# Optimization experiments

Measured on AMD Instinct MI355X. Metric: run time of the kernel, lower is better.

## Reference

```python
import jax, jax.numpy as jnp
import numpy as np

B = 64
H_FS = W_FS = 56
IN_DIM, OUT_DIM, NUM_HEADS = 96, 192, 2
HEAD_DIM = OUT_DIM // NUM_HEADS  # 96
STRIDE_Q, STRIDE_KV = (2, 2), (4, 4)
REL_RANGE = 2 * (H_FS // STRIDE_Q[0]) - 1  # 55
LN_EPS = 1e-5


def setup_inputs() -> dict:
    key = jax.random.key(0)
    ks = jax.random.split(key, 12)
    N = H_FS * W_FS + 1  # +1 cls token
    s = 0.02
    d = {
        "hidden_states": jax.random.normal(ks[0], (B, N, IN_DIM), jnp.float32),
        "Wq": jax.random.normal(ks[1], (IN_DIM, OUT_DIM), jnp.float32) * s,
        "bq": jnp.zeros((OUT_DIM,), jnp.float32),
        "Wk": jax.random.normal(ks[2], (IN_DIM, OUT_DIM), jnp.float32) * s,
        "bk": jnp.zeros((OUT_DIM,), jnp.float32),
        "Wv": jax.random.normal(ks[3], (IN_DIM, OUT_DIM), jnp.float32) * s,
        "bv": jnp.zeros((OUT_DIM,), jnp.float32),
        # depthwise pool convs: (C_out=C, C_in/groups=1, kh, kw)
        "pool_q_w": jax.random.normal(ks[4], (IN_DIM, 1, 3, 3), jnp.float32) * 0.1,
        "pool_k_w": jax.random.normal(ks[5], (IN_DIM, 1, 3, 3), jnp.float32) * 0.1,
        "pool_v_w": jax.random.normal(ks[6], (IN_DIM, 1, 3, 3), jnp.float32) * 0.1,
        "gq": jnp.ones((IN_DIM,), jnp.float32), "betaq": jnp.zeros((IN_DIM,), jnp.float32),
        "gk": jnp.ones((IN_DIM,), jnp.float32), "betak": jnp.zeros((IN_DIM,), jnp.float32),
        "gv": jnp.ones((IN_DIM,), jnp.float32), "betav": jnp.zeros((IN_DIM,), jnp.float32),
        "rel_h": jax.random.normal(ks[7], (REL_RANGE, HEAD_DIM), jnp.float32) * s,
        "rel_w": jax.random.normal(ks[8], (REL_RANGE, HEAD_DIM), jnp.float32) * s,
        "height": H_FS,
        "width": W_FS,
    }
    return d


def _layernorm(x, g, b):
    m = x.mean(-1, keepdims=True)
    v = ((x - m) ** 2).mean(-1, keepdims=True)
    return (x - m) * jax.lax.rsqrt(v + LN_EPS) * g + b


def _pool(x, w, stride, g, b, height, width):
    # x: (B, folds=1, N, C) with cls token first
    bsz, _, _, C = x.shape
    cls_tok, rest = x[:, :, :1], x[:, :, 1:]
    sp = rest.reshape(bsz, height, width, C).transpose(0, 3, 1, 2)  # (B, C, H, W)
    y = jax.lax.conv_general_dilated(
        sp, w, stride, [(1, 1), (1, 1)], feature_group_count=C,
        dimension_numbers=("NCHW", "OIHW", "NCHW"))
    hp, wp = y.shape[2], y.shape[3]
    y = y.reshape(bsz, 1, C, hp * wp).transpose(0, 1, 3, 2)  # (B, 1, N', C)
    y = jnp.concatenate([cls_tok, y], axis=2)
    return _layernorm(y, g, b), (hp, wp)


def _rel_idx(qn, kn):
    q_ratio = max(kn / qn, 1.0)
    k_ratio = max(qn / kn, 1.0)
    dist = (np.arange(qn)[:, None] * q_ratio - np.arange(kn)[None, :] * k_ratio
            + (kn - 1) * k_ratio)
    return dist.astype(np.int64)


def reference(hidden_states, Wq, bq, Wk, bk, Wv, bv, pool_q_w, pool_k_w, pool_v_w,
              gq, betaq, gk, betak, gv, betav, rel_h, rel_w, height, width):
    bsz, N, C = hidden_states.shape
    h = hidden_states.reshape(bsz, N, 1, C).transpose(0, 2, 1, 3)  # (B, folds=1, N, C)

    q, (qh, qw) = _pool(h, pool_q_w, STRIDE_Q, gq, betaq, height, width)
    k, (kh, kw) = _pool(h, pool_k_w, STRIDE_KV, gk, betak, height, width)
    v, _ = _pool(h, pool_v_w, STRIDE_KV, gv, betav, height, width)

    def proj(x, W, bias, n):
        x = x.transpose(0, 2, 1, 3).reshape(bsz, n, -1)
        x = x @ W + bias
        return x.reshape(bsz, n, NUM_HEADS, HEAD_DIM).transpose(0, 2, 1, 3)

    nq, nk = qh * qw + 1, kh * kw + 1
    q = proj(q, Wq, bq, nq)  # (B, H, nq, d)
    k = proj(k, Wk, bk, nk)
    v = proj(v, Wv, bv, nk)

    scale = HEAD_DIM ** -0.5
    attn = jnp.einsum("bhqd,bhkd->bhqk", q * scale, k)

    # decomposed spatial relative positional bias (cls offset = 1)
    Rh = rel_h[_rel_idx(qh, kh)]  # (qh, kh, d)
    Rw = rel_w[_rel_idx(qw, kw)]  # (qw, kw, d)
    rq = q[:, :, 1:].reshape(bsz, NUM_HEADS, qh, qw, HEAD_DIM)
    eh = jnp.einsum("byhwc,hkc->byhwk", rq, Rh)
    ew = jnp.einsum("byhwc,wkc->byhwk", rq, Rw)
    blk = (attn[:, :, 1:, 1:].reshape(bsz, NUM_HEADS, qh, qw, kh, kw)
           + eh[..., :, None] + ew[..., None, :])
    attn = attn.at[:, :, 1:, 1:].set(blk.reshape(bsz, NUM_HEADS, qh * qw, kh * kw))

    attn = jax.nn.softmax(attn, axis=-1)
    out = jnp.einsum("bhqk,bhkd->bhqd", attn, v)
    out = out.at[:, :, 1:].add(q[:, :, 1:])  # residual pooling (skip cls)
    return out.transpose(0, 2, 1, 3).reshape(bsz, nq, OUT_DIM)
```

## Files before the change

kernel.cpp:

```cpp
#include <hip/hip_runtime.h>
#include <hip/hip_bf16.h>
#include <hip/hip_fp16.h>

#define B_    64
#define HFS   56
#define CIN   96
#define NQ    785
#define NK    197
#define QW    28
#define KW    14
#define NTOT  3137
#define NQP   800
#define NKP   208
#define NKPV  224
#define VROWS 112
#define KSCL  0.10206207261596575f
#define LOG2E 1.4426950408889634f
#define KSCL2 (KSCL*LOG2E)

typedef __attribute__((ext_vector_type(8))) short short8;
typedef __attribute__((ext_vector_type(4))) short shortx4;
typedef __attribute__((ext_vector_type(4))) float floatx4;

__device__ __forceinline__ short f2s(float x) {
    __hip_bfloat16 h = __float2bfloat16(x);
    return *reinterpret_cast<short*>(&h);
}
__device__ __forceinline__ float s2f(short s) {
    __hip_bfloat16 h; *reinterpret_cast<short*>(&h) = s;
    return __bfloat162float(h);
}
__device__ __forceinline__ short8 ld8(const short* p) {
    return *reinterpret_cast<const short8*>(p);
}
__device__ __forceinline__ unsigned pkbf(float a, float b) {
    return (unsigned)(unsigned short)f2s(a) | ((unsigned)(unsigned short)f2s(b) << 16);
}
__device__ __forceinline__ unsigned pkhf(float a, float b) {
    __half2 h = __floats2half2_rn(a, b);
    return *reinterpret_cast<unsigned*>(&h);
}
__device__ __forceinline__ float hflo(unsigned w) {
    __half2 h = *reinterpret_cast<__half2*>(&w);
    return __half2float(__low2half(h));
}
__device__ __forceinline__ float hfhi(unsigned w) {
    __half2 h = *reinterpret_cast<__half2*>(&w);
    return __half2float(__high2half(h));
}

#define MFMA16(a,b,c) __builtin_amdgcn_mfma_f32_16x16x32_bf16((a),(b),(c),0,0,0)

__global__ void prep_kernel(const float* __restrict__ Wq, const float* __restrict__ Wk,
                            const float* __restrict__ Wv, const float* __restrict__ relh,
                            const float* __restrict__ relw,
                            const float* __restrict__ pqw, const float* __restrict__ pkw,
                            const float* __restrict__ pvw,
                            short* __restrict__ WTq, short* __restrict__ WTk,
                            short* __restrict__ WTv, short* __restrict__ relc,
                            short* __restrict__ vt,
                            float* __restrict__ cwqT, float* __restrict__ cwkT,
                            float* __restrict__ cwvT)
{
    int i = blockIdx.x * 256 + threadIdx.x;
    if (i < 18432)      { int o = i/96, c = i%96;              WTq[o*96+c] = f2s(Wq[c*192+o]); }
    else if (i < 36864) { int j = i-18432; int o=j/96,c=j%96;  WTk[o*96+c] = f2s(Wk[c*192+o]*KSCL2); }
    else if (i < 55296) { int j = i-36864; int o=j/96,c=j%96;  WTv[o*96+c] = f2s(Wv[c*192+o]); }
    else if (i < 66048) {
        int j = i - 55296;  int r = j/96, c = j%96;
        float v = (r < 54) ? relh[r*96+c] : ((r < 108) ? relw[(r-54)*96+c] : 0.f);
        relc[r*96+c] = f2s(v*LOG2E);
    } else if (i < 721408) {
        int j2 = i - 66048;
        int bh = j2 / 5120, r = j2 % 5120;
        int row, tok; short val;
        if (r < 3584) { row = 96 + r/224; tok = r%224;
                        val = (row == 96 && tok < NK) ? (short)0x3F80 : (short)0; }
        else          { int rr = r-3584; row = rr/16; tok = 208 + (rr%16); val = 0; }
        vt[((long)bh*VROWS + row)*NKPV + tok] = val;
    } else if (i < 724000) {
        int j = i - 721408;
        int w = j / 864, r = j % 864;
        int c = r / 9, off = r % 9;
        const float* src = (w == 0) ? pqw : (w == 1) ? pkw : pvw;
        float*       dst = (w == 0) ? cwqT : (w == 1) ? cwkT : cwvT;
        dst[off*96 + c] = src[c*9 + off];
    }
}

__device__ __forceinline__ void red16_2(float& s, float& ss) {
    #pragma unroll
    for (int off = 8; off >= 1; off >>= 1) {
        s  += __shfl_xor(s,  off, 16);
        ss += __shfl_xor(ss, off, 16);
    }
}

__device__ __forceinline__ void ln6_store(const float* x, float m, float r,
    const float* __restrict__ g, const float* __restrict__ beta,
    int c0, short* __restrict__ outp)
{
    float2 g0 = *reinterpret_cast<const float2*>(g + c0);
    float2 g1 = *reinterpret_cast<const float2*>(g + c0 + 2);
    float2 g2 = *reinterpret_cast<const float2*>(g + c0 + 4);
    float2 b0 = *reinterpret_cast<const float2*>(beta + c0);
    float2 b1 = *reinterpret_cast<const float2*>(beta + c0 + 2);
    float2 b2 = *reinterpret_cast<const float2*>(beta + c0 + 4);
    unsigned o0 = pkbf((x[0]-m)*r*g0.x + b0.x, (x[1]-m)*r*g0.y + b0.y);
    unsigned o1 = pkbf((x[2]-m)*r*g1.x + b1.x, (x[3]-m)*r*g1.y + b1.y);
    unsigned o2 = pkbf((x[4]-m)*r*g2.x + b2.x, (x[5]-m)*r*g2.y + b2.y);
    *reinterpret_cast<unsigned*>(outp)     = o0;
    *reinterpret_cast<unsigned*>(outp + 2) = o1;
    *reinterpret_cast<unsigned*>(outp + 4) = o2;
}

__device__ __forceinline__ void zero6(short* __restrict__ outp) {
    *reinterpret_cast<unsigned*>(outp)     = 0u;
    *reinterpret_cast<unsigned*>(outp + 2) = 0u;
    *reinterpret_cast<unsigned*>(outp + 4) = 0u;
}

__global__ __launch_bounds__(256) void pool_ln_kernel(
    const float* __restrict__ hs,
    const float* __restrict__ cwqT, const float* __restrict__ cwkT, const float* __restrict__ cwvT,
    const float* __restrict__ gq, const float* __restrict__ betaq,
    const float* __restrict__ gk, const float* __restrict__ betak,
    const float* __restrict__ gv, const float* __restrict__ betav,
    short* __restrict__ pq, short* __restrict__ pk, short* __restrict__ pv)
{
    const int wid  = threadIdx.x >> 6;
    const int lane = threadIdx.x & 63;
    const int sub  = lane >> 4;
    const int li   = lane & 15;
    const int c0   = li * 6;
    const int gid  = blockIdx.x * 4 + wid;
    const int b    = gid / 252;
    const int slot = gid % 252;
    const long hb  = (long)b * NTOT * CIN;

    if (slot < 200) {
        int t = slot*4 + sub;
        short* outp = pq + ((long)b*NQP + t)*CIN + c0;
        if (t >= NQ) { zero6(outp); return; }
        float x[6];
        #pragma unroll
        for (int i = 0; i < 6; ++i) x[i] = 0.f;
        if (t == 0) {
            const float* hp = hs + hb + c0;
            float2 a0 = *reinterpret_cast<const float2*>(hp);
            float2 a1 = *reinterpret_cast<const float2*>(hp + 2);
            float2 a2 = *reinterpret_cast<const float2*>(hp + 4);
            x[0]=a0.x; x[1]=a0.y; x[2]=a1.x; x[3]=a1.y; x[4]=a2.x; x[5]=a2.y;
        } else {
            int j = t - 1, oy = j / QW, ox = j % QW;
            float2 hbuf[9][3];
            #pragma unroll
            for (int tap = 0; tap < 9; ++tap) {
                int dy = tap / 3, dx = tap % 3;
                int iy = oy*2 - 1 + dy;
                int ix = ox*2 - 1 + dx;
                if (iy >= 0 && iy < HFS && ix >= 0 && ix < HFS) {
                    const float* hp = hs + hb + (long)(1 + iy*HFS + ix)*CIN + c0;
                    hbuf[tap][0] = *reinterpret_cast<const float2*>(hp);
                    hbuf[tap][1] = *reinterpret_cast<const float2*>(hp + 2);
                    hbuf[tap][2] = *reinterpret_cast<const float2*>(hp + 4);
                } else {
                    hbuf[tap][0] = float2{0.f, 0.f};
                    hbuf[tap][1] = float2{0.f, 0.f};
                    hbuf[tap][2] = float2{0.f, 0.f};
                }
            }
            #pragma unroll
            for (int tap = 0; tap < 9; ++tap) {
                const float* wp = cwqT + tap*96 + c0;
                float2 w0 = *reinterpret_cast<const float2*>(wp);
                float2 w1 = *reinterpret_cast<const float2*>(wp + 2);
                float2 w2 = *reinterpret_cast<const float2*>(wp + 4);
                x[0] = fmaf(hbuf[tap][0].x, w0.x, x[0]); x[1] = fmaf(hbuf[tap][0].y, w0.y, x[1]);
                x[2] = fmaf(hbuf[tap][1].x, w1.x, x[2]); x[3] = fmaf(hbuf[tap][1].y, w1.y, x[3]);
                x[4] = fmaf(hbuf[tap][2].x, w2.x, x[4]); x[5] = fmaf(hbuf[tap][2].y, w2.y, x[5]);
            }
        }
        float s  = (x[0]+x[1]) + (x[2]+x[3]) + (x[4]+x[5]);
        float ss = fmaf(x[0],x[0], fmaf(x[1],x[1], fmaf(x[2],x[2],
                   fmaf(x[3],x[3], fmaf(x[4],x[4], x[5]*x[5])))));
        red16_2(s, ss);
        float m   = s * (1.f/96.f);
        float var = ss * (1.f/96.f) - m*m;
        float r   = rsqrtf(var + 1e-5f);
        ln6_store(x, m, r, gq, betaq, c0, outp);
    } else {
        int tok = (slot - 200)*4 + sub;
        short* ok_ = pk + ((long)b*NKP + tok)*CIN + c0;
        short* ov_ = pv + ((long)b*NKP + tok)*CIN + c0;
        if (tok >= NK) { zero6(ok_); zero6(ov_); return; }
        float xk[6], xv[6];
        #pragma unroll
        for (int i = 0; i < 6; ++i) { xk[i] = 0.f; xv[i] = 0.f; }
        if (tok == 0) {
            const float* hp = hs + hb + c0;
            float2 a0 = *reinterpret_cast<const float2*>(hp);
            float2 a1 = *reinterpret_cast<const float2*>(hp + 2);
            float2 a2 = *reinterpret_cast<const float2*>(hp + 4);
            xk[0]=xv[0]=a0.x; xk[1]=xv[1]=a0.y; xk[2]=xv[2]=a1.x;
            xk[3]=xv[3]=a1.y; xk[4]=xv[4]=a2.x; xk[5]=xv[5]=a2.y;
        } else {
            int j = tok - 1, oy = j / KW, ox = j % KW;
            float2 hbuf[9][3];
            #pragma unroll
            for (int tap = 0; tap < 9; ++tap) {
                int dy = tap / 3, dx = tap % 3;
                int iy = oy*4 - 1 + dy;
                int ix = ox*4 - 1 + dx;
                if (iy >= 0 && iy < HFS && ix >= 0 && ix < HFS) {
                    const float* hp = hs + hb + (long)(1 + iy*HFS + ix)*CIN + c0;
                    hbuf[tap][0] = *reinterpret_cast<const float2*>(hp);
                    hbuf[tap][1] = *reinterpret_cast<const float2*>(hp + 2);
                    hbuf[tap][2] = *reinterpret_cast<const float2*>(hp + 4);
                } else {
                    hbuf[tap][0] = float2{0.f, 0.f};
                    hbuf[tap][1] = float2{0.f, 0.f};
                    hbuf[tap][2] = float2{0.f, 0.f};
                }
            }
            #pragma unroll
            for (int tap = 0; tap < 9; ++tap) {
                int wo = tap*96 + c0;
                float2 k0 = *reinterpret_cast<const float2*>(cwkT + wo);
                float2 k1 = *reinterpret_cast<const float2*>(cwkT + wo + 2);
                float2 k2 = *reinterpret_cast<const float2*>(cwkT + wo + 4);
                float2 v0 = *reinterpret_cast<const float2*>(cwvT + wo);
                float2 v1 = *reinterpret_cast<const float2*>(cwvT + wo + 2);
                float2 v2 = *reinterpret_cast<const float2*>(cwvT + wo + 4);
                xk[0] = fmaf(hbuf[tap][0].x, k0.x, xk[0]); xk[1] = fmaf(hbuf[tap][0].y, k0.y, xk[1]);
                xk[2] = fmaf(hbuf[tap][1].x, k1.x, xk[2]); xk[3] = fmaf(hbuf[tap][1].y, k1.y, xk[3]);
                xk[4] = fmaf(hbuf[tap][2].x, k2.x, xk[4]); xk[5] = fmaf(hbuf[tap][2].y, k2.y, xk[5]);
                xv[0] = fmaf(hbuf[tap][0].x, v0.x, xv[0]); xv[1] = fmaf(hbuf[tap][0].y, v0.y, xv[1]);
                xv[2] = fmaf(hbuf[tap][1].x, v1.x, xv[2]); xv[3] = fmaf(hbuf[tap][1].y, v1.y, xv[3]);
                xv[4] = fmaf(hbuf[tap][2].x, v2.x, xv[4]); xv[5] = fmaf(hbuf[tap][2].y, v2.y, xv[5]);
            }
        }
        float sk  = (xk[0]+xk[1]) + (xk[2]+xk[3]) + (xk[4]+xk[5]);
        float ssk = fmaf(xk[0],xk[0], fmaf(xk[1],xk[1], fmaf(xk[2],xk[2],
                    fmaf(xk[3],xk[3], fmaf(xk[4],xk[4], xk[5]*xk[5])))));
        float sv  = (xv[0]+xv[1]) + (xv[2]+xv[3]) + (xv[4]+xv[5]);
        float ssv = fmaf(xv[0],xv[0], fmaf(xv[1],xv[1], fmaf(xv[2],xv[2],
                    fmaf(xv[3],xv[3], fmaf(xv[4],xv[4], xv[5]*xv[5])))));
        red16_2(sk, ssk);
        red16_2(sv, ssv);
        float mk = sk * (1.f/96.f), vark = ssk * (1.f/96.f) - mk*mk;
        float mv = sv * (1.f/96.f), varv = ssv * (1.f/96.f) - mv*mv;
        float rk = rsqrtf(vark + 1e-5f);
        float rv = rsqrtf(varv + 1e-5f);
        ln6_store(xk, mk, rk, gk, betak, c0, ok_);
        ln6_store(xv, mv, rv, gv, betav, c0, ov_);
    }
}

__global__ __launch_bounds__(256) void proj_mfma_kernel(
    const short* __restrict__ pq, const short* __restrict__ pk, const short* __restrict__ pv,
    const short* __restrict__ WTq, const short* __restrict__ WTk, const short* __restrict__ WTv,
    const float* __restrict__ bq, const float* __restrict__ bk, const float* __restrict__ bv,
    short* __restrict__ qb, short* __restrict__ kb, short* __restrict__ vt)
{
    int wid  = threadIdx.x >> 6;
    int lane = threadIdx.x & 63;
    int quad = lane >> 4, col = lane & 15;
    int wt = blockIdx.x * 4 + wid;

    if (wt < 1008) {
        const short *A, *WT; const float* bias; short* outp;
        int ntokp, row0; float bsc;
        if (wt < 800) { A = pq; WT = WTq; bias = bq; outp = qb; ntokp = NQP; row0 = wt*64; bsc = 1.f; }
        else          { A = pk; WT = WTk; bias = bk; outp = kb; ntokp = NKP; row0 = (wt-800)*64; bsc = KSCL2; }

        short8 bt[4][3];
        #pragma unroll
        for (int ti = 0; ti < 4; ++ti)
            #pragma unroll
            for (int cc = 0; cc < 3; ++cc)
                bt[ti][cc] = ld8(A + (long)(row0 + ti*16 + col)*96 + cc*32 + quad*8);

        int bT[4], tokT[4];
        #pragma unroll
        for (int ti = 0; ti < 4; ++ti) {
            int r = row0 + ti*16;
            bT[ti] = r / ntokp;
            tokT[ti] = (r % ntokp) + col;
        }

        short8 af[2][3];
        #pragma unroll
        for (int cc = 0; cc < 3; ++cc)
            af[0][cc] = ld8(WT + col*96 + cc*32 + quad*8);

        #pragma unroll
        for (int nt = 0; nt < 12; ++nt) {
            if (nt < 11) {
                #pragma unroll
                for (int cc = 0; cc < 3; ++cc)
                    af[(nt+1)&1][cc] = ld8(WT + ((nt+1)*16 + col)*96 + cc*32 + quad*8);
            }
            int o0 = nt*16 + quad*4;
            float4 bo = *reinterpret_cast<const float4*>(bias + o0);
            int h  = (o0 >= 96) ? 1 : 0;
            int d0 = o0 - h*96;
            #pragma unroll
            for (int ti = 0; ti < 4; ++ti) {
                floatx4 acc = {0.f, 0.f, 0.f, 0.f};
                #pragma unroll
                for (int cc = 0; cc < 3; ++cc)
                    acc = MFMA16(af[nt&1][cc], bt[ti][cc], acc);
                shortx4 val;
                val.x = f2s(acc[0] + bo.x*bsc);
                val.y = f2s(acc[1] + bo.y*bsc);
                val.z = f2s(acc[2] + bo.z*bsc);
                val.w = f2s(acc[3] + bo.w*bsc);
                *reinterpret_cast<shortx4*>(outp + ((long)(bT[ti]*2 + h)*ntokp + tokT[ti])*96 + d0) = val;
            }
        }
    } else {
        int row0 = (wt - 1008) * 64;
        short8 at[4][3];
        #pragma unroll
        for (int ti = 0; ti < 4; ++ti)
            #pragma unroll
            for (int cc = 0; cc < 3; ++cc)
                at[ti][cc] = ld8(pv + (long)(row0 + ti*16 + col)*96 + cc*32 + quad*8);

        int bT[4], t0T[4];
        #pragma unroll
        for (int ti = 0; ti < 4; ++ti) {
            int r = row0 + ti*16;
            bT[ti] = r / NKP;
            t0T[ti] = (r % NKP) + quad*4;
        }

        short8 bf[2][3];
        #pragma unroll
        for (int cc = 0; cc < 3; ++cc)
            bf[0][cc] = ld8(WTv + col*96 + cc*32 + quad*8);

        #pragma unroll
        for (int nt = 0; nt < 12; ++nt) {
            if (nt < 11) {
                #pragma unroll
                for (int cc = 0; cc < 3; ++cc)
                    bf[(nt+1)&1][cc] = ld8(WTv + ((nt+1)*16 + col)*96 + cc*32 + quad*8);
            }
            int o = nt*16 + col;
            int h = (o >= 96) ? 1 : 0;
            int d = o - h*96;
            float bo = bv[o];
            #pragma unroll
            for (int ti = 0; ti < 4; ++ti) {
                floatx4 acc = {0.f, 0.f, 0.f, 0.f};
                #pragma unroll
                for (int cc = 0; cc < 3; ++cc)
                    acc = MFMA16(at[ti][cc], bf[nt&1][cc], acc);
                shortx4 val;
                val.x = (t0T[ti]+0 < NK) ? f2s(acc[0] + bo) : (short)0;
                val.y = (t0T[ti]+1 < NK) ? f2s(acc[1] + bo) : (short)0;
                val.z = (t0T[ti]+2 < NK) ? f2s(acc[2] + bo) : (short)0;
                val.w = (t0T[ti]+3 < NK) ? f2s(acc[3] + bo) : (short)0;
                *reinterpret_cast<shortx4*>(vt + ((long)(bT[ti]*2 + h)*VROWS + d)*NKPV + t0T[ti]) = val;
            }
        }
    }
}

__global__ __launch_bounds__(64, 2) void attn_kernel(
    const short* __restrict__ qb, const short* __restrict__ kb,
    const short* __restrict__ vt, const short* __restrict__ relc,
    float* __restrict__ out)
{
    __shared__ __align__(16) short smem[2][16][232];

    int lane = threadIdx.x & 63;
    int quad = lane >> 4, col = lane & 15;

    int bid = blockIdx.x;
    int wt  = (bid & 7) * 400 + (bid >> 3);
    int bh  = wt / 25;
    int tp  = wt % 25;
    int q0  = tp * 32;

    const short* qrow = qb + ((long)bh*NQP + q0)*96;
    short8 aq[2][3];
    #pragma unroll
    for (int ti = 0; ti < 2; ++ti)
        #pragma unroll
        for (int c = 0; c < 3; ++c)
            aq[ti][c] = ld8(qrow + (ti*16 + col)*96 + c*32 + quad*8);

    short8 rf[2][3];
    #pragma unroll
    for (int c = 0; c < 3; ++c)
        rf[0][c] = ld8(relc + col*96 + c*32 + quad*8);
    #pragma unroll
    for (int rt = 0; rt < 7; ++rt) {
        if (rt < 6) {
            #pragma unroll
            for (int c = 0; c < 3; ++c)
                rf[(rt+1)&1][c] = ld8(relc + ((rt+1)*16 + col)*96 + c*32 + quad*8);
        }
        #pragma unroll
        for (int ti = 0; ti < 2; ++ti) {
            floatx4 acc = {0.f, 0.f, 0.f, 0.f};
            #pragma unroll
            for (int c = 0; c < 3; ++c)
                acc = MFMA16(aq[ti][c], rf[rt&1][c], acc);
            #pragma unroll
            for (int reg = 0; reg < 4; ++reg)
                smem[ti][quad*4 + reg][rt*16 + col] = f2s(acc[reg]);
        }
    }

    const short* kbase = kb + (long)bh*NKP*96;
    short8 kf[3][3];
    #pragma unroll
    for (int c = 0; c < 3; ++c)
        kf[0][c] = ld8(kbase + col*96 + c*32 + quad*8);
    #pragma unroll
    for (int c = 0; c < 3; ++c)
        kf[1][c] = ld8(kbase + (16 + col)*96 + c*32 + quad*8);

    int qyo[2][4], qxo[2][4];
    #pragma unroll
    for (int ti = 0; ti < 2; ++ti)
        #pragma unroll
        for (int reg = 0; reg < 4; ++reg) {
            int qq = q0 + ti*16 + quad*4 + reg;
            int jj = (qq > 0) ? (qq - 1) : 0;
            qyo[ti][reg] = jj / QW;
            qxo[ti][reg] = jj % QW;
        }

    unsigned bpk[2][13][2];
    #pragma unroll
    for (int kt = 0; kt < 13; ++kt) {
        int k  = kt*16 + col;
        int kk = (k > 0) ? (k - 1) : 0;
        int ky = kk / 14;  ky = (ky < 13) ? ky : 13;
        int kx = kk - 14*ky;
        int oh  = 26 - 2*ky;
        int ow2 = 26 - 2*kx;
        #pragma unroll
        for (int ti = 0; ti < 2; ++ti) {
            float bs[4];
            #pragma unroll
            for (int reg = 0; reg < 4; ++reg) {
                const short* er = &smem[ti][quad*4 + reg][0];
                float bias = s2f(er[qyo[ti][reg] + oh]) + s2f(er[54 + qxo[ti][reg] + ow2]);
                if (kt == 0) bias = (col == 0) ? 0.f : bias;
                if (q0 == 0 && ti == 0 && reg == 0) bias = (quad == 0) ? 0.f : bias;
                bs[reg] = bias;
            }
            bpk[ti][kt][0] = pkhf(bs[0], bs[1]);
            bpk[ti][kt][1] = pkhf(bs[2], bs[3]);
        }
    }

    const short* vbase = vt + (long)bh*VROWS*NKPV;
    short8 vf[2][7];
    #pragma unroll
    for (int kt = 0; kt < 13; ++kt) {
        if (kt < 11) {
            #pragma unroll
            for (int c = 0; c < 3; ++c)
                kf[(kt+2)%3][c] = ld8(kbase + ((kt+2)*16 + col)*96 + c*32 + quad*8);
        } else if (kt == 11) {
            #pragma unroll
            for (int nt = 0; nt < 7; ++nt)
                vf[0][nt] = ld8(vbase + (nt*16 + col)*NKPV + quad*8);
        }
        int k = kt*16 + col;
        __builtin_amdgcn_s_setprio(1);
        floatx4 accA = {0.f, 0.f, 0.f, 0.f};
        floatx4 accB = {0.f, 0.f, 0.f, 0.f};
        #pragma unroll
        for (int c = 0; c < 3; ++c) {
            accA = MFMA16(aq[0][c], kf[kt%3][c], accA);
            accB = MFMA16(aq[1][c], kf[kt%3][c], accB);
        }
        __builtin_amdgcn_s_setprio(0);
        unsigned a0 = bpk[0][kt][0], a1 = bpk[0][kt][1];
        unsigned b0 = bpk[1][kt][0], b1 = bpk[1][kt][1];
        smem[0][quad*4 + 0][k] = f2s(__builtin_amdgcn_exp2f(accA[0] + hflo(a0)));
        smem[0][quad*4 + 1][k] = f2s(__builtin_amdgcn_exp2f(accA[1] + hfhi(a0)));
        smem[0][quad*4 + 2][k] = f2s(__builtin_amdgcn_exp2f(accA[2] + hflo(a1)));
        smem[0][quad*4 + 3][k] = f2s(__builtin_amdgcn_exp2f(accA[3] + hfhi(a1)));
        smem[1][quad*4 + 0][k] = f2s(__builtin_amdgcn_exp2f(accB[0] + hflo(b0)));
        smem[1][quad*4 + 1][k] = f2s(__builtin_amdgcn_exp2f(accB[1] + hfhi(b0)));
        smem[1][quad*4 + 2][k] = f2s(__builtin_amdgcn_exp2f(accB[2] + hflo(b1)));
        smem[1][quad*4 + 3][k] = f2s(__builtin_amdgcn_exp2f(accB[3] + hfhi(b1)));
    }
    #pragma unroll
    for (int ti = 0; ti < 2; ++ti)
        #pragma unroll
        for (int reg = 0; reg < 4; ++reg)
            smem[ti][quad*4 + reg][208 + col] = 0;

    floatx4 o[2][7];
    #pragma unroll
    for (int ti = 0; ti < 2; ++ti)
        #pragma unroll
        for (int nt = 0; nt < 7; ++nt) o[ti][nt] = floatx4{0.f, 0.f, 0.f, 0.f};
    #pragma unroll
    for (int c = 0; c < 7; ++c) {
        if (c < 6) {
            #pragma unroll
            for (int nt = 0; nt < 7; ++nt)
                vf[(c+1)&1][nt] = ld8(vbase + (nt*16 + col)*NKPV + (c+1)*32 + quad*8);
        }
        short8 apA = ld8(&smem[0][col][c*32 + quad*8]);
        short8 apB = ld8(&smem[1][col][c*32 + quad*8]);
        __builtin_amdgcn_s_setprio(1);
        #pragma unroll
        for (int nt = 0; nt < 7; ++nt) {
            o[0][nt] = MFMA16(apA, vf[c&1][nt], o[0][nt]);
            o[1][nt] = MFMA16(apB, vf[c&1][nt], o[1][nt]);
        }
        __builtin_amdgcn_s_setprio(0);
    }

    float inv[2][4];
    #pragma unroll
    for (int ti = 0; ti < 2; ++ti)
        #pragma unroll
        for (int reg = 0; reg < 4; ++reg) {
            float srow = __shfl(o[ti][6][reg], lane & 48, 64);
            inv[ti][reg] = 1.0f / srow;
        }

    float* fsm = reinterpret_cast<float*>(&smem[0][0][0]);
    #pragma unroll
    for (int ti = 0; ti < 2; ++ti)
        #pragma unroll
        for (int nt = 0; nt < 6; ++nt)
            #pragma unroll
            for (int reg = 0; reg < 4; ++reg)
                fsm[(ti*16 + quad*4 + reg)*102 + nt*16 + col] = o[ti][nt][reg] * inv[ti][reg];

    int b = bh >> 1, h = bh & 1;
    int r2  = lane >> 1;
    int h2  = lane & 1;
    int ti2 = r2 >> 4, row2 = r2 & 15;
    int q   = q0 + ti2*16 + row2;
    int ch0 = h2 * 48;
    if (q < NQ) {
        const float* src  = fsm + (ti2*16 + row2)*102 + ch0;
        const short* resp = qb + ((long)bh*NQP + q)*96 + ch0;
        float*       outp = out + ((long)b*NQ + q)*192 + h*96 + ch0;
        #pragma unroll
        for (int i = 0; i < 6; ++i) {
            float2 v0 = *reinterpret_cast<const float2*>(src + i*8 + 0);
            float2 v1 = *reinterpret_cast<const float2*>(src + i*8 + 2);
            float2 v2 = *reinterpret_cast<const float2*>(src + i*8 + 4);
            float2 v3 = *reinterpret_cast<const float2*>(src + i*8 + 6);
            float r_[8];
            if (q > 0) {
                short8 rs = ld8(resp + i*8);
                #pragma unroll
                for (int j = 0; j < 8; ++j) r_[j] = s2f(rs[j]);
            } else {
                #pragma unroll
                for (int j = 0; j < 8; ++j) r_[j] = 0.f;
            }
            float4 o0, o1;
            o0.x = v0.x + r_[0]; o0.y = v0.y + r_[1];
            o0.z = v1.x + r_[2]; o0.w = v1.y + r_[3];
            o1.x = v2.x + r_[4]; o1.y = v2.y + r_[5];
            o1.z = v3.x + r_[6]; o1.w = v3.y + r_[7];
            *reinterpret_cast<float4*>(outp + i*8)     = o0;
            *reinterpret_cast<float4*>(outp + i*8 + 4) = o1;
        }
    }
}

extern "C" void kernel_launch(void* const* d_in, const int* in_sizes, int n_in,
                              void* d_out, int out_size, void* d_ws, size_t ws_size,
                              hipStream_t stream)
{
    const float* hs    = (const float*)d_in[0];
    const float* Wq    = (const float*)d_in[1];
    const float* bq    = (const float*)d_in[2];
    const float* Wk    = (const float*)d_in[3];
    const float* bk    = (const float*)d_in[4];
    const float* Wv    = (const float*)d_in[5];
    const float* bv    = (const float*)d_in[6];
    const float* pqw   = (const float*)d_in[7];
    const float* pkw   = (const float*)d_in[8];
    const float* pvw   = (const float*)d_in[9];
    const float* gq    = (const float*)d_in[10];
    const float* betaq = (const float*)d_in[11];
    const float* gk    = (const float*)d_in[12];
    const float* betak = (const float*)d_in[13];
    const float* gv    = (const float*)d_in[14];
    const float* betav = (const float*)d_in[15];
    const float* relh  = (const float*)d_in[16];
    const float* relw  = (const float*)d_in[17];
    float* out = (float*)d_out;

    short* pq   = (short*)d_ws;
    short* pk   = pq  + (long)B_*NQP*CIN;
    short* pv   = pk  + (long)B_*NKP*CIN;
    short* qb   = pv  + (long)B_*NKP*CIN;
    short* kb   = qb  + (long)128*NQP*96;
    short* vt   = kb  + (long)128*NKP*96;
    short* WTq  = vt  + (long)128*VROWS*NKPV;
    short* WTk  = WTq + 192*96;
    short* WTv  = WTk + 192*96;
    short* relc = WTv + 192*96;
    float* cwqT = (float*)(relc + 112*96);
    float* cwkT = cwqT + 9*96;
    float* cwvT = cwkT + 9*96;

    prep_kernel<<<2829, 256, 0, stream>>>(Wq, Wk, Wv, relh, relw,
                                          pqw, pkw, pvw,
                                          WTq, WTk, WTv, relc, vt,
                                          cwqT, cwkT, cwvT);

    pool_ln_kernel<<<(B_*1008)/16, 256, 0, stream>>>(
        hs, cwqT, cwkT, cwvT, gq, betaq, gk, betak, gv, betav, pq, pk, pv);

    proj_mfma_kernel<<<1216/4, 256, 0, stream>>>(
        pq, pk, pv, WTq, WTk, WTv, bq, bk, bv, qb, kb, vt);

    attn_kernel<<<3200, 64, 0, stream>>>(qb, kb, vt, relc, out);
}
```

Baseline: 233.9 us.

## Fold weight prep into pool kernel and widen pool/LN loads to 8 channels

The large prep kernel is split up. The conv-weight transpose stays in a tiny 11-block kernel, while the projection-weight transpose, relative-bias conversion and vt padding init move into extra blocks appended to the pool/LN launch. The vt init now writes short8 vectors instead of single shorts. The pool/LN path switches from 6 channels per lane to 8 channels with float4 loads and 16-byte stores, leaving 4 of every 16 lanes idle. The aim is to cut launch count and per-element memory ops, at the cost of lane underutilisation and some divergence in the pool kernel.

```diff
diff --git a/kernel.cpp b/kernel.cpp
--- a/kernel.cpp
+++ b/kernel.cpp
@@ -21,6 +21,7 @@
 typedef __attribute__((ext_vector_type(8))) short short8;
 typedef __attribute__((ext_vector_type(4))) short shortx4;
 typedef __attribute__((ext_vector_type(4))) float floatx4;
+typedef __attribute__((ext_vector_type(4))) unsigned uintx4;
 
 __device__ __forceinline__ short f2s(float x) {
     __hip_bfloat16 h = __float2bfloat16(x);
@@ -51,36 +52,14 @@
 
 #define MFMA16(a,b,c) __builtin_amdgcn_mfma_f32_16x16x32_bf16((a),(b),(c),0,0,0)
 
-__global__ void prep_kernel(const float* __restrict__ Wq, const float* __restrict__ Wk,
-                            const float* __restrict__ Wv, const float* __restrict__ relh,
-                            const float* __restrict__ relw,
-                            const float* __restrict__ pqw, const float* __restrict__ pkw,
-                            const float* __restrict__ pvw,
-                            short* __restrict__ WTq, short* __restrict__ WTk,
-                            short* __restrict__ WTv, short* __restrict__ relc,
-                            short* __restrict__ vt,
-                            float* __restrict__ cwqT, float* __restrict__ cwkT,
-                            float* __restrict__ cwvT)
+__global__ void prep_w_kernel(const float* __restrict__ pqw, const float* __restrict__ pkw,
+                              const float* __restrict__ pvw,
+                              float* __restrict__ cwqT, float* __restrict__ cwkT,
+                              float* __restrict__ cwvT)
 {
     int i = blockIdx.x * 256 + threadIdx.x;
-    if (i < 18432)      { int o = i/96, c = i%96;              WTq[o*96+c] = f2s(Wq[c*192+o]); }
-    else if (i < 36864) { int j = i-18432; int o=j/96,c=j%96;  WTk[o*96+c] = f2s(Wk[c*192+o]*KSCL2); }
-    else if (i < 55296) { int j = i-36864; int o=j/96,c=j%96;  WTv[o*96+c] = f2s(Wv[c*192+o]); }
-    else if (i < 66048) {
-        int j = i - 55296;  int r = j/96, c = j%96;
-        float v = (r < 54) ? relh[r*96+c] : ((r < 108) ? relw[(r-54)*96+c] : 0.f);
-        relc[r*96+c] = f2s(v*LOG2E);
-    } else if (i < 721408) {
-        int j2 = i - 66048;
-        int bh = j2 / 5120, r = j2 % 5120;
-        int row, tok; short val;
-        if (r < 3584) { row = 96 + r/224; tok = r%224;
-                        val = (row == 96 && tok < NK) ? (short)0x3F80 : (short)0; }
-        else          { int rr = r-3584; row = rr/16; tok = 208 + (rr%16); val = 0; }
-        vt[((long)bh*VROWS + row)*NKPV + tok] = val;
-    } else if (i < 724000) {
-        int j = i - 721408;
-        int w = j / 864, r = j % 864;
+    if (i < 2592) {
+        int w = i / 864, r = i % 864;
         int c = r / 9, off = r % 9;
         const float* src = (w == 0) ? pqw : (w == 1) ? pkw : pvw;
         float*       dst = (w == 0) ? cwqT : (w == 1) ? cwkT : cwvT;
@@ -96,28 +75,25 @@
     }
 }
 
-__device__ __forceinline__ void ln6_store(const float* x, float m, float r,
+__device__ __forceinline__ void ln8_store(const float* x, float m, float r,
     const float* __restrict__ g, const float* __restrict__ beta,
     int c0, short* __restrict__ outp)
 {
-    float2 g0 = *reinterpret_cast<const float2*>(g + c0);
-    float2 g1 = *reinterpret_cast<const float2*>(g + c0 + 2);
-    float2 g2 = *reinterpret_cast<const float2*>(g + c0 + 4);
-    float2 b0 = *reinterpret_cast<const float2*>(beta + c0);
-    float2 b1 = *reinterpret_cast<const float2*>(beta + c0 + 2);
-    float2 b2 = *reinterpret_cast<const float2*>(beta + c0 + 4);
-    unsigned o0 = pkbf((x[0]-m)*r*g0.x + b0.x, (x[1]-m)*r*g0.y + b0.y);
-    unsigned o1 = pkbf((x[2]-m)*r*g1.x + b1.x, (x[3]-m)*r*g1.y + b1.y);
-    unsigned o2 = pkbf((x[4]-m)*r*g2.x + b2.x, (x[5]-m)*r*g2.y + b2.y);
-    *reinterpret_cast<unsigned*>(outp)     = o0;
-    *reinterpret_cast<unsigned*>(outp + 2) = o1;
-    *reinterpret_cast<unsigned*>(outp + 4) = o2;
-}
-
-__device__ __forceinline__ void zero6(short* __restrict__ outp) {
-    *reinterpret_cast<unsigned*>(outp)     = 0u;
-    *reinterpret_cast<unsigned*>(outp + 2) = 0u;
-    *reinterpret_cast<unsigned*>(outp + 4) = 0u;
+    float4 g0 = *reinterpret_cast<const float4*>(g + c0);
+    float4 g1 = *reinterpret_cast<const float4*>(g + c0 + 4);
+    float4 b0 = *reinterpret_cast<const float4*>(beta + c0);
+    float4 b1 = *reinterpret_cast<const float4*>(beta + c0 + 4);
+    uintx4 v;
+    v.x = pkbf((x[0]-m)*r*g0.x + b0.x, (x[1]-m)*r*g0.y + b0.y);
+    v.y = pkbf((x[2]-m)*r*g0.z + b0.z, (x[3]-m)*r*g0.w + b0.w);
+    v.z = pkbf((x[4]-m)*r*g1.x + b1.x, (x[5]-m)*r*g1.y + b1.y);
+    v.w = pkbf((x[6]-m)*r*g1.z + b1.z, (x[7]-m)*r*g1.w + b1.w);
+    *reinterpret_cast<uintx4*>(outp + c0) = v;
+}
+
+__device__ __forceinline__ void zero8(short* __restrict__ outp, int c0) {
+    uintx4 v = {0u, 0u, 0u, 0u};
+    *reinterpret_cast<uintx4*>(outp + c0) = v;
 }
 
 __global__ __launch_bounds__(256) void pool_ln_kernel(
@@ -126,13 +102,50 @@
     const float* __restrict__ gq, const float* __restrict__ betaq,
     const float* __restrict__ gk, const float* __restrict__ betak,
     const float* __restrict__ gv, const float* __restrict__ betav,
-    short* __restrict__ pq, short* __restrict__ pk, short* __restrict__ pv)
+    short* __restrict__ pq, short* __restrict__ pk, short* __restrict__ pv,
+    const float* __restrict__ Wq, const float* __restrict__ Wk, const float* __restrict__ Wv,
+    const float* __restrict__ relh, const float* __restrict__ relw,
+    short* __restrict__ WTq, short* __restrict__ WTk, short* __restrict__ WTv,
+    short* __restrict__ relc, short* __restrict__ vt)
 {
+    if (blockIdx.x >= 4032) {
+        int i = (blockIdx.x - 4032) * 256 + threadIdx.x;
+        if (i < 18432)      { int o = i/96, c = i%96;              WTq[o*96+c] = f2s(Wq[c*192+o]); }
+        else if (i < 36864) { int j = i-18432; int o=j/96,c=j%96;  WTk[o*96+c] = f2s(Wk[c*192+o]*KSCL2); }
+        else if (i < 55296) { int j = i-36864; int o=j/96,c=j%96;  WTv[o*96+c] = f2s(Wv[c*192+o]); }
+        else if (i < 66048) {
+            int j = i - 55296;  int r = j/96, c = j%96;
+            float v = (r < 54) ? relh[r*96+c] : ((r < 108) ? relw[(r-54)*96+c] : 0.f);
+            relc[r*96+c] = f2s(v*LOG2E);
+        } else {
+            int j2 = i - 66048;
+            int bh = j2 / 640, r = (j2 % 640) * 8;
+            short8 val = {0,0,0,0,0,0,0,0};
+            long addr;
+            if (r < 3584) {
+                int row = 96 + r/224, tok0 = r%224;
+                if (row == 96) {
+                    #pragma unroll
+                    for (int t = 0; t < 8; ++t)
+                        val[t] = (tok0 + t < NK) ? (short)0x3F80 : (short)0;
+                }
+                addr = ((long)bh*VROWS + row)*NKPV + tok0;
+            } else {
+                int rr = r - 3584;
+                int row = rr/16, tok0 = 208 + (rr%16);
+                addr = ((long)bh*VROWS + row)*NKPV + tok0;
+            }
+            *reinterpret_cast<short8*>(vt + addr) = val;
+        }
+        return;
+    }
+
     const int wid  = threadIdx.x >> 6;
     const int lane = threadIdx.x & 63;
     const int sub  = lane >> 4;
     const int li   = lane & 15;
-    const int c0   = li * 6;
+    const bool ACT = (li < 12);
+    const int c0   = li * 8;
     const int gid  = blockIdx.x * 4 + wid;
     const int b    = gid / 252;
     const int slot = gid % 252;
@@ -140,120 +153,118 @@
 
     if (slot < 200) {
         int t = slot*4 + sub;
-        short* outp = pq + ((long)b*NQP + t)*CIN + c0;
-        if (t >= NQ) { zero6(outp); return; }
-        float x[6];
-        #pragma unroll
-        for (int i = 0; i < 6; ++i) x[i] = 0.f;
-        if (t == 0) {
-            const float* hp = hs + hb + c0;
-            float2 a0 = *reinterpret_cast<const float2*>(hp);
-            float2 a1 = *reinterpret_cast<const float2*>(hp + 2);
-            float2 a2 = *reinterpret_cast<const float2*>(hp + 4);
-            x[0]=a0.x; x[1]=a0.y; x[2]=a1.x; x[3]=a1.y; x[4]=a2.x; x[5]=a2.y;
-        } else {
-            int j = t - 1, oy = j / QW, ox = j % QW;
-            float2 hbuf[9][3];
-            #pragma unroll
-            for (int tap = 0; tap < 9; ++tap) {
-                int dy = tap / 3, dx = tap % 3;
-                int iy = oy*2 - 1 + dy;
-                int ix = ox*2 - 1 + dx;
-                if (iy >= 0 && iy < HFS && ix >= 0 && ix < HFS) {
-                    const float* hp = hs + hb + (long)(1 + iy*HFS + ix)*CIN + c0;
-                    hbuf[tap][0] = *reinterpret_cast<const float2*>(hp);
-                    hbuf[tap][1] = *reinterpret_cast<const float2*>(hp + 2);
-                    hbuf[tap][2] = *reinterpret_cast<const float2*>(hp + 4);
-                } else {
-                    hbuf[tap][0] = float2{0.f, 0.f};
-                    hbuf[tap][1] = float2{0.f, 0.f};
-                    hbuf[tap][2] = float2{0.f, 0.f};
+        short* outp = pq + ((long)b*NQP + t)*CIN;
+        if (t >= NQ) { if (ACT) zero8(outp, c0); return; }
+        float x[8];
+        #pragma unroll
+        for (int i = 0; i < 8; ++i) x[i] = 0.f;
+        if (ACT) {
+            if (t == 0) {
+                float4 a0 = *reinterpret_cast<const float4*>(hs + hb + c0);
+                float4 a1 = *reinterpret_cast<const float4*>(hs + hb + c0 + 4);
+                x[0]=a0.x; x[1]=a0.y; x[2]=a0.z; x[3]=a0.w;
+                x[4]=a1.x; x[5]=a1.y; x[6]=a1.z; x[7]=a1.w;
+            } else {
+                int j = t - 1, oy = j / QW, ox = j % QW;
+                float4 hbuf[9][2];
+                #pragma unroll
+                for (int tap = 0; tap < 9; ++tap) {
+                    int dy = tap / 3, dx = tap % 3;
+                    int iy = oy*2 - 1 + dy;
+                    int ix = ox*2 - 1 + dx;
+                    if (iy >= 0 && iy < HFS && ix >= 0 && ix < HFS) {
+                        const float* hp = hs + hb + (long)(1 + iy*HFS + ix)*CIN + c0;
+                        hbuf[tap][0] = *reinterpret_cast<const float4*>(hp);
+                        hbuf[tap][1] = *reinterpret_cast<const float4*>(hp + 4);
+                    } else {
+                        hbuf[tap][0] = float4{0.f,0.f,0.f,0.f};
+                        hbuf[tap][1] = float4{0.f,0.f,0.f,0.f};
+                    }
                 }
-            }
-            #pragma unroll
-            for (int tap = 0; tap < 9; ++tap) {
-                const float* wp = cwqT + tap*96 + c0;
-                float2 w0 = *reinterpret_cast<const float2*>(wp);
-                float2 w1 = *reinterpret_cast<const float2*>(wp + 2);
-                float2 w2 = *reinterpret_cast<const float2*>(wp + 4);
-                x[0] = fmaf(hbuf[tap][0].x, w0.x, x[0]); x[1] = fmaf(hbuf[tap][0].y, w0.y, x[1]);
-                x[2] = fmaf(hbuf[tap][1].x, w1.x, x[2]); x[3] = fmaf(hbuf[tap][1].y, w1.y, x[3]);
-                x[4] = fmaf(hbuf[tap][2].x, w2.x, x[4]); x[5] = fmaf(hbuf[tap][2].y, w2.y, x[5]);
-            }
-        }
-        float s  = (x[0]+x[1]) + (x[2]+x[3]) + (x[4]+x[5]);
-        float ss = fmaf(x[0],x[0], fmaf(x[1],x[1], fmaf(x[2],x[2],
-                   fmaf(x[3],x[3], fmaf(x[4],x[4], x[5]*x[5])))));
+                #pragma unroll
+                for (int tap = 0; tap < 9; ++tap) {
+                    float4 w0 = *reinterpret_cast<const float4*>(cwqT + tap*96 + c0);
+                    float4 w1 = *reinterpret_cast<const float4*>(cwqT + tap*96 + c0 + 4);
+                    x[0] = fmaf(hbuf[tap][0].x, w0.x, x[0]); x[1] = fmaf(hbuf[tap][0].y, w0.y, x[1]);
+                    x[2] = fmaf(hbuf[tap][0].z, w0.z, x[2]); x[3] = fmaf(hbuf[tap][0].w, w0.w, x[3]);
+                    x[4] = fmaf(hbuf[tap][1].x, w1.x, x[4]); x[5] = fmaf(hbuf[tap][1].y, w1.y, x[5]);
+                    x[6] = fmaf(hbuf[tap][1].z, w1.z, x[6]); x[7] = fmaf(hbuf[tap][1].w, w1.w, x[7]);
+                }
+            }
+        }
+        float s  = ((x[0]+x[1]) + (x[2]+x[3])) + ((x[4]+x[5]) + (x[6]+x[7]));
+        float ss = fmaf(x[0],x[0], fmaf(x[1],x[1], fmaf(x[2],x[2], fmaf(x[3],x[3],
+                   fmaf(x[4],x[4], fmaf(x[5],x[5], fmaf(x[6],x[6], x[7]*x[7])))))));
         red16_2(s, ss);
         float m   = s * (1.f/96.f);
         float var = ss * (1.f/96.f) - m*m;
         float r   = rsqrtf(var + 1e-5f);
-        ln6_store(x, m, r, gq, betaq, c0, outp);
+        if (ACT) ln8_store(x, m, r, gq, betaq, c0, outp);
     } else {
         int tok = (slot - 200)*4 + sub;
-        short* ok_ = pk + ((long)b*NKP + tok)*CIN + c0;
-        short* ov_ = pv + ((long)b*NKP + tok)*CIN + c0;
-        if (tok >= NK) { zero6(ok_); zero6(ov_); return; }
-        float xk[6], xv[6];
-        #pragma unroll
-        for (int i = 0; i < 6; ++i) { xk[i] = 0.f; xv[i] = 0.f; }
-        if (tok == 0) {
-            const float* hp = hs + hb + c0;
-            float2 a0 = *reinterpret_cast<const float2*>(hp);
-            float2 a1 = *reinterpret_cast<const float2*>(hp + 2);
-            float2 a2 = *reinterpret_cast<const float2*>(hp + 4);
-            xk[0]=xv[0]=a0.x; xk[1]=xv[1]=a0.y; xk[2]=xv[2]=a1.x;
-            xk[3]=xv[3]=a1.y; xk[4]=xv[4]=a2.x; xk[5]=xv[5]=a2.y;
-        } else {
-            int j = tok - 1, oy = j / KW, ox = j % KW;
-            float2 hbuf[9][3];
-            #pragma unroll
-            for (int tap = 0; tap < 9; ++tap) {
-                int dy = tap / 3, dx = tap % 3;
-                int iy = oy*4 - 1 + dy;
-                int ix = ox*4 - 1 + dx;
-                if (iy >= 0 && iy < HFS && ix >= 0 && ix < HFS) {
-                    const float* hp = hs + hb + (long)(1 + iy*HFS + ix)*CIN + c0;
-                    hbuf[tap][0] = *reinterpret_cast<const float2*>(hp);
-                    hbuf[tap][1] = *reinterpret_cast<const float2*>(hp + 2);
-                    hbuf[tap][2] = *reinterpret_cast<const float2*>(hp + 4);
-                } else {
-                    hbuf[tap][0] = float2{0.f, 0.f};
-                    hbuf[tap][1] = float2{0.f, 0.f};
-                    hbuf[tap][2] = float2{0.f, 0.f};
+        short* ok_ = pk + ((long)b*NKP + tok)*CIN;
+        short* ov_ = pv + ((long)b*NKP + tok)*CIN;
+        if (tok >= NK) { if (ACT) { zero8(ok_, c0); zero8(ov_, c0); } return; }
+        float xk[8], xv[8];
+        #pragma unroll
+        for (int i = 0; i < 8; ++i) { xk[i] = 0.f; xv[i] = 0.f; }
+        if (ACT) {
+            if (tok == 0) {
+                float4 a0 = *reinterpret_cast<const float4*>(hs + hb + c0);
+                float4 a1 = *reinterpret_cast<const float4*>(hs + hb + c0 + 4);
+                xk[0]=xv[0]=a0.x; xk[1]=xv[1]=a0.y; xk[2]=xv[2]=a0.z; xk[3]=xv[3]=a0.w;
+                xk[4]=xv[4]=a1.x; xk[5]=xv[5]=a1.y; xk[6]=xv[6]=a1.z; xk[7]=xv[7]=a1.w;
+            } else {
+                int j = tok - 1, oy = j / KW, ox = j % KW;
+                float4 hbuf[9][2];
+                #pragma unroll
+                for (int tap = 0; tap < 9; ++tap) {
+                    int dy = tap / 3, dx = tap % 3;
+                    int iy = oy*4 - 1 + dy;
+                    int ix = ox*4 - 1 + dx;
+                    if (iy >= 0 && iy < HFS && ix >= 0 && ix < HFS) {
+                        const float* hp = hs + hb + (long)(1 + iy*HFS + ix)*CIN + c0;
+                        hbuf[tap][0] = *reinterpret_cast<const float4*>(hp);
+                        hbuf[tap][1] = *reinterpret_cast<const float4*>(hp + 4);
+                    } else {
+                        hbuf[tap][0] = float4{0.f,0.f,0.f,0.f};
+                        hbuf[tap][1] = float4{0.f,0.f,0.f,0.f};
+                    }
                 }
-            }
-            #pragma unroll
-            for (int tap = 0; tap < 9; ++tap) {
-                int wo = tap*96 + c0;
-                float2 k0 = *reinterpret_cast<const float2*>(cwkT + wo);
-                float2 k1 = *reinterpret_cast<const float2*>(cwkT + wo + 2);
-                float2 k2 = *reinterpret_cast<const float2*>(cwkT + wo + 4);
-                float2 v0 = *reinterpret_cast<const float2*>(cwvT + wo);
-                float2 v1 = *reinterpret_cast<const float2*>(cwvT + wo + 2);
-                float2 v2 = *reinterpret_cast<const float2*>(cwvT + wo + 4);
-                xk[0] = fmaf(hbuf[tap][0].x, k0.x, xk[0]); xk[1] = fmaf(hbuf[tap][0].y, k0.y, xk[1]);
-                xk[2] = fmaf(hbuf[tap][1].x, k1.x, xk[2]); xk[3] = fmaf(hbuf[tap][1].y, k1.y, xk[3]);
-                xk[4] = fmaf(hbuf[tap][2].x, k2.x, xk[4]); xk[5] = fmaf(hbuf[tap][2].y, k2.y, xk[5]);
-                xv[0] = fmaf(hbuf[tap][0].x, v0.x, xv[0]); xv[1] = fmaf(hbuf[tap][0].y, v0.y, xv[1]);
-                xv[2] = fmaf(hbuf[tap][1].x, v1.x, xv[2]); xv[3] = fmaf(hbuf[tap][1].y, v1.y, xv[3]);
-                xv[4] = fmaf(hbuf[tap][2].x, v2.x, xv[4]); xv[5] = fmaf(hbuf[tap][2].y, v2.y, xv[5]);
-            }
-        }
-        float sk  = (xk[0]+xk[1]) + (xk[2]+xk[3]) + (xk[4]+xk[5]);
-        float ssk = fmaf(xk[0],xk[0], fmaf(xk[1],xk[1], fmaf(xk[2],xk[2],
-                    fmaf(xk[3],xk[3], fmaf(xk[4],xk[4], xk[5]*xk[5])))));
-        float sv  = (xv[0]+xv[1]) + (xv[2]+xv[3]) + (xv[4]+xv[5]);
-        float ssv = fmaf(xv[0],xv[0], fmaf(xv[1],xv[1], fmaf(xv[2],xv[2],
-                    fmaf(xv[3],xv[3], fmaf(xv[4],xv[4], xv[5]*xv[5])))));
+                #pragma unroll
+                for (int tap = 0; tap < 9; ++tap) {
+                    int wo = tap*96 + c0;
+                    float4 k0 = *reinterpret_cast<const float4*>(cwkT + wo);
+                    float4 k1 = *reinterpret_cast<const float4*>(cwkT + wo + 4);
+                    float4 v0 = *reinterpret_cast<const float4*>(cwvT + wo);
+                    float4 v1 = *reinterpret_cast<const float4*>(cwvT + wo + 4);
+                    xk[0] = fmaf(hbuf[tap][0].x, k0.x, xk[0]); xk[1] = fmaf(hbuf[tap][0].y, k0.y, xk[1]);
+                    xk[2] = fmaf(hbuf[tap][0].z, k0.z, xk[2]); xk[3] = fmaf(hbuf[tap][0].w, k0.w, xk[3]);
+                    xk[4] = fmaf(hbuf[tap][1].x, k1.x, xk[4]); xk[5] = fmaf(hbuf[tap][1].y, k1.y, xk[5]);
+                    xk[6] = fmaf(hbuf[tap][1].z, k1.z, xk[6]); xk[7] = fmaf(hbuf[tap][1].w, k1.w, xk[7]);
+                    xv[0] = fmaf(hbuf[tap][0].x, v0.x, xv[0]); xv[1] = fmaf(hbuf[tap][0].y, v0.y, xv[1]);
+                    xv[2] = fmaf(hbuf[tap][0].z, v0.z, xv[2]); xv[3] = fmaf(hbuf[tap][0].w, v0.w, xv[3]);
+                    xv[4] = fmaf(hbuf[tap][1].x, v1.x, xv[4]); xv[5] = fmaf(hbuf[tap][1].y, v1.y, xv[5]);
+                    xv[6] = fmaf(hbuf[tap][1].z, v1.z, xv[6]); xv[7] = fmaf(hbuf[tap][1].w, v1.w, xv[7]);
+                }
+            }
+        }
+        float sk  = ((xk[0]+xk[1]) + (xk[2]+xk[3])) + ((xk[4]+xk[5]) + (xk[6]+xk[7]));
+        float ssk = fmaf(xk[0],xk[0], fmaf(xk[1],xk[1], fmaf(xk[2],xk[2], fmaf(xk[3],xk[3],
+                    fmaf(xk[4],xk[4], fmaf(xk[5],xk[5], fmaf(xk[6],xk[6], xk[7]*xk[7])))))));
+        float sv  = ((xv[0]+xv[1]) + (xv[2]+xv[3])) + ((xv[4]+xv[5]) + (xv[6]+xv[7]));
+        float ssv = fmaf(xv[0],xv[0], fmaf(xv[1],xv[1], fmaf(xv[2],xv[2], fmaf(xv[3],xv[3],
+                    fmaf(xv[4],xv[4], fmaf(xv[5],xv[5], fmaf(xv[6],xv[6], xv[7]*xv[7])))))));
         red16_2(sk, ssk);
         red16_2(sv, ssv);
         float mk = sk * (1.f/96.f), vark = ssk * (1.f/96.f) - mk*mk;
         float mv = sv * (1.f/96.f), varv = ssv * (1.f/96.f) - mv*mv;
         float rk = rsqrtf(vark + 1e-5f);
         float rv = rsqrtf(varv + 1e-5f);
-        ln6_store(xk, mk, rk, gk, betak, c0, ok_);
-        ln6_store(xv, mv, rv, gv, betav, c0, ov_);
+        if (ACT) {
+            ln8_store(xk, mk, rk, gk, betak, c0, ok_);
+            ln8_store(xv, mv, rv, gv, betav, c0, ov_);
+        }
     }
 }
 
@@ -616,13 +627,11 @@
     float* cwkT = cwqT + 9*96;
     float* cwvT = cwkT + 9*96;
 
-    prep_kernel<<<2829, 256, 0, stream>>>(Wq, Wk, Wv, relh, relw,
-                                          pqw, pkw, pvw,
-                                          WTq, WTk, WTv, relc, vt,
-                                          cwqT, cwkT, cwvT);
-
-    pool_ln_kernel<<<(B_*1008)/16, 256, 0, stream>>>(
-        hs, cwqT, cwkT, cwvT, gq, betaq, gk, betak, gv, betav, pq, pk, pv);
+    prep_w_kernel<<<11, 256, 0, stream>>>(pqw, pkw, pvw, cwqT, cwkT, cwvT);
+
+    pool_ln_kernel<<<4032 + 578, 256, 0, stream>>>(
+        hs, cwqT, cwkT, cwvT, gq, betaq, gk, betak, gv, betav, pq, pk, pv,
+        Wq, Wk, Wv, relh, relw, WTq, WTk, WTv, relc, vt);
 
     proj_mfma_kernel<<<1216/4, 256, 0, stream>>>(
         pq, pk, pv, WTq, WTk, WTv, bq, bk, bv, qb, kb, vt);
```

Measured after the change: 231.2 us. No clear change (-1.2%).
